# Performance work log

Measured on AMD Instinct MI355X. Metric: run time of the kernel, lower is better.

Reference implementation:

```python
import jax, jax.numpy as jnp
import numpy as np

N_HEADS = 16


def _rope(x, cos, sin):
    # x: (B,H,S,hd); cos,sin: (1,1,S,hd//2). Full-dim rotation (rot_dim == head_dim).
    xe = x[..., 0::2]
    xo = x[..., 1::2]
    re = xe * cos - xo * sin
    ro = xe * sin + xo * cos
    return jnp.stack([re, ro], axis=-1).reshape(x.shape)


def setup_inputs() -> dict:
    key = jax.random.key(0)
    B, S, D = 2, 2048, 1024
    hd = D // N_HEADS
    k1, k2, k3, k4, k5 = jax.random.split(key, 5)
    x = jax.random.normal(k1, (B, S, D), dtype=jnp.float32)
    # Linear params (lecun-normal-ish scale)
    w_qkv = jax.random.normal(k2, (D, 3 * D), dtype=jnp.float32) / np.sqrt(D)
    b_qkv = jnp.zeros((3 * D,), dtype=jnp.float32)
    w_out = jax.random.normal(k3, (D, D), dtype=jnp.float32) / np.sqrt(D)
    b_out = jnp.zeros((D,), dtype=jnp.float32)
    # Rotary tables: (S, hd//2)
    inv_freq = 1.0 / (10000.0 ** (np.arange(0, hd, 2, dtype=np.float32) / hd))
    angles = jnp.asarray(np.arange(S, dtype=np.float32)[:, None] * inv_freq[None, :])
    cos = jnp.cos(angles)
    sin = jnp.sin(angles)
    # Causal mask (seq, seq), True = attend
    mask = jnp.tril(jnp.ones((S, S), dtype=bool))
    return {"x": x, "w_qkv": w_qkv, "b_qkv": b_qkv, "w_out": w_out,
            "b_out": b_out, "cos": cos, "sin": sin, "mask": mask}


def reference(x, w_qkv, b_qkv, w_out, b_out, cos, sin, mask):
    B, S, D = x.shape
    H = N_HEADS
    hd = D // H
    scale = hd ** (-0.5)
    qkv = x @ w_qkv + b_qkv  # (B,S,3D)
    qkv = qkv.reshape(B, S, 3, H, hd).transpose(2, 0, 3, 1, 4)  # (3,B,H,S,hd)
    q, k, v = qkv[0], qkv[1], qkv[2]
    c = cos[None, None, :, :]
    s = sin[None, None, :, :]
    q = _rope(q, c, s)
    k = _rope(k, c, s)
    attn = jnp.einsum('bhqd,bhkd->bhqk', q, k) * scale
    attn = jnp.where(mask, attn, -1e9)
    attn = jax.nn.softmax(attn, axis=-1)
    out = jnp.einsum('bhqk,bhkd->bhqd', attn, v)
    out = out.transpose(0, 2, 1, 3).reshape(B, S, D)
    return out @ w_out + b_out
```

## Files before the change

kernel.cpp:

```cpp
#include <hip/hip_runtime.h>
#include <stdint.h>

typedef unsigned short u16;
typedef __attribute__((ext_vector_type(8))) __bf16 bf16x8;
typedef __attribute__((ext_vector_type(4))) float f32x4;
typedef __attribute__((ext_vector_type(4))) unsigned short u16x4;

__device__ __forceinline__ float bf2f(u16 u){
  unsigned int x = ((unsigned int)u) << 16;
  return __builtin_bit_cast(float, x);
}
__device__ __forceinline__ u16 f2bf(float f){
  return __builtin_bit_cast(u16, (__bf16)f);
}
__device__ __forceinline__ float fexp2(float x){ return __builtin_exp2f(x); }
__device__ __forceinline__ void lds_load16(const void* g, void* l){
  __builtin_amdgcn_global_load_lds(
      (const __attribute__((address_space(1))) unsigned int*)g,
      (__attribute__((address_space(3))) unsigned int*)l, 16, 0, 0);
}

__device__ __forceinline__ void transpose_body(const float* __restrict__ in,
                                               u16* __restrict__ out,
                                               int R, int C, int bx, int by,
                                               u16 (*t)[65]){
  const int c0 = bx * 64, r0 = by * 64;
  const int tid = threadIdx.x;
  const int rr = tid >> 3;
  const int cc = (tid & 7) * 8;
#pragma unroll
  for (int i = 0; i < 2; i++){
    int r = i * 32 + rr;
    const float* p = in + (size_t)(r0 + r) * C + c0 + cc;
    f32x4 v0 = *(const f32x4*)p;
    f32x4 v1 = *(const f32x4*)(p + 4);
#pragma unroll
    for (int j = 0; j < 4; j++){ t[r][cc + j] = f2bf(v0[j]); t[r][cc + 4 + j] = f2bf(v1[j]); }
  }
  __syncthreads();
#pragma unroll
  for (int i = 0; i < 2; i++){
    int c = i * 32 + rr;
    u16 tmp[8];
#pragma unroll
    for (int j = 0; j < 8; j++) tmp[j] = t[cc + j][c];
    *(bf16x8*)(out + (size_t)(c0 + c) * R + r0 + cc) = *(const bf16x8*)tmp;
  }
}

__global__ __launch_bounds__(256) void prep(const float* __restrict__ w_qkv,
                                            const float* __restrict__ w_out,
                                            const float* __restrict__ x,
                                            u16* __restrict__ wT1,
                                            u16* __restrict__ wT2,
                                            u16* __restrict__ xbf){
  __shared__ u16 t[64][65];
  const int bid = blockIdx.x;
  if (bid < 2048){
    int i = bid * 256 + threadIdx.x;
    const float* p = x + (size_t)i * 8;
    f32x4 v0 = *(const f32x4*)p;
    f32x4 v1 = *(const f32x4*)(p + 4);
    u16 tmp[8];
#pragma unroll
    for (int j = 0; j < 4; j++){ tmp[j] = f2bf(v0[j]); tmp[4 + j] = f2bf(v1[j]); }
    *(bf16x8*)(xbf + (size_t)i * 8) = *(const bf16x8*)tmp;
  } else if (bid < 2048 + 768){
    int idx = bid - 2048;
    transpose_body(w_qkv, wT1, 1024, 3072, idx % 48, idx / 48, t);
  } else {
    int idx = bid - 2816;
    transpose_body(w_out, wT2, 1024, 1024, idx % 16, idx / 16, t);
  }
}

__global__ __launch_bounds__(256) void v_transpose(const u16* __restrict__ qkv,
                                                   u16* __restrict__ vT){
  const int S = 2048, LD = 3072;
  __shared__ u16 t[64][65];
  const int bh = blockIdx.y;
  const int b = bh >> 4, h = bh & 15;
  const int s0 = blockIdx.x * 64;
  const u16* src = qkv + (size_t)b * S * LD + 2048 + h * 64;
  const int tid = threadIdx.x;
  const int rr = tid >> 3;
  const int cc = (tid & 7) * 8;
#pragma unroll
  for (int i = 0; i < 2; i++){
    int s = i * 32 + rr;
    bf16x8 v = *(const bf16x8*)(src + (size_t)(s0 + s) * LD + cc);
#pragma unroll
    for (int j = 0; j < 8; j++) t[s][cc + j] = __builtin_bit_cast(u16, (__bf16)v[j]);
  }
  __syncthreads();
  u16* dst = vT + (size_t)bh * 64 * S;
#pragma unroll
  for (int i = 0; i < 2; i++){
    int d = i * 32 + rr;
    u16 tmp[8];
#pragma unroll
    for (int j = 0; j < 8; j++) tmp[j] = t[cc + j][d];
    *(bf16x8*)(dst + (size_t)d * S + s0 + cc) = *(const bf16x8*)tmp;
  }
}

#define GSTAGE(P_, K0_)                                                        \
  { _Pragma("unroll")                                                          \
    for (int i = 0; i < 2; i++){                                               \
      int row0 = i * 64 + w * 16;                                              \
      int row = row0 + lrow;                                                   \
      int cs = lcd ^ ((row >> 1) & 3);                                         \
      lds_load16(A  + (size_t)(bm * 128 + row) * K + (K0_) + cs * 8,           \
                 (char*)As + (P_) * 8192 + row0 * 64);                         \
      lds_load16(Bt + (size_t)(bn * 128 + row) * K + (K0_) + cs * 8,           \
                 (char*)Bs + (P_) * 8192 + row0 * 64);                         \
    } }

template<bool OUTF32, bool ROPE>
__global__ __launch_bounds__(256, 3) void gemm_bt(const u16* __restrict__ A,
                                                  const u16* __restrict__ Bt,
                                                  const float* __restrict__ bias,
                                                  void* __restrict__ Cv,
                                                  int M, int N, int K,
                                                  const float* __restrict__ cosb,
                                                  const float* __restrict__ sinb,
                                                  u16* __restrict__ vTo){
  __shared__ u16 smem[16384];
  u16* As = smem;
  u16* Bs = smem + 8192;
  const int nx = gridDim.x;
  const int L = blockIdx.x + nx * blockIdx.y;
  const int per = (nx * gridDim.y) >> 3;
  const int wg = (L & 7) * per + (L >> 3);
  const int bn = wg % nx, bm = wg / nx;
  const int tid = threadIdx.x, w = tid >> 6, l = tid & 63;
  const int lo = l & 15, hi = l >> 4;
  const int wr = (w >> 1) * 64, wc = (w & 1) * 64;
  f32x4 acc[4][4] = {};
  const int lrow = l >> 2, lcd = l & 3;

  GSTAGE(0, 0);
  __syncthreads();
  for (int k0 = 0; k0 < K; k0 += 32){
    const int p = (k0 >> 5) & 1;
    if (k0 + 32 < K) GSTAGE(p ^ 1, k0 + 32);
    bf16x8 a[4], b[4];
#pragma unroll
    for (int mi = 0; mi < 4; mi++){
      int row = wr + mi * 16 + lo;
      unsigned byte = (unsigned)(row * 64 + hi * 16) ^ (((row >> 1) & 3) << 4);
      a[mi] = *(const bf16x8*)((const char*)As + p * 8192 + byte);
    }
#pragma unroll
    for (int ni = 0; ni < 4; ni++){
      int row = wc + ni * 16 + lo;
      unsigned byte = (unsigned)(row * 64 + hi * 16) ^ (((row >> 1) & 3) << 4);
      b[ni] = *(const bf16x8*)((const char*)Bs + p * 8192 + byte);
    }
    __builtin_amdgcn_s_setprio(1);
#pragma unroll
    for (int mi = 0; mi < 4; mi++)
#pragma unroll
      for (int ni = 0; ni < 4; ni++)
        acc[mi][ni] = __builtin_amdgcn_mfma_f32_16x16x32_bf16(a[mi], b[ni], acc[mi][ni], 0, 0, 0);
    __builtin_amdgcn_s_setprio(0);
    __syncthreads();
  }
  if (ROPE && bn < 16){
#pragma unroll
    for (int mi = 0; mi < 4; mi++){
#pragma unroll
      for (int r = 0; r < 4; r++){
        int grow = bm * 128 + wr + mi * 16 + hi * 4 + r;
        int stok = grow & 2047;
#pragma unroll
        for (int ni = 0; ni < 4; ni++){
          int col = bn * 128 + wc + ni * 16 + lo;
          float v = acc[mi][ni][r] + bias[col];
          float partner = __shfl_xor(v, 1, 64);
          int ip = (col & 63) >> 1;
          float c = cosb[stok * 32 + ip], sn = sinb[stok * 32 + ip];
          float res = (lo & 1) ? (partner * sn + v * c) : (v * c - partner * sn);
          ((u16*)Cv)[(size_t)grow * N + col] = f2bf(res);
        }
      }
    }
  } else if (ROPE && vTo != nullptr){
    const int bloc = (bm * 128) >> 11;
    const int s0g  = (bm * 128) & 2047;
#pragma unroll
    for (int H = 0; H < 2; H++){
      if ((w & 1) == H){
#pragma unroll
        for (int mi = 0; mi < 4; mi++){
#pragma unroll
          for (int ni = 0; ni < 4; ni++){
            int d = ni * 16 + lo;
            int col = bn * 128 + wc + ni * 16 + lo;
            int sb = wr + mi * 16 + hi * 4;
            u16x4 pk;
#pragma unroll
            for (int r = 0; r < 4; r++) pk[r] = f2bf(acc[mi][ni][r] + bias[col]);
            *(u16x4*)&smem[d * 128 + (sb ^ ((d & 15) << 3))] = pk;
          }
        }
      }
      __syncthreads();
      int hh = (bn - 16) * 2 + H;
      u16* dst = vTo + (size_t)(bloc * 16 + hh) * 64 * 2048;
#pragma unroll
      for (int i = 0; i < 4; i++){
        int c = tid + 256 * i;
        int d = c >> 4, sc = c & 15;
        bf16x8 v = *(const bf16x8*)&smem[d * 128 + ((sc * 8) ^ ((d & 15) << 3))];
        *(bf16x8*)(dst + (size_t)d * 2048 + s0g + sc * 8) = v;
      }
      __syncthreads();
    }
  } else {
#pragma unroll
    for (int mi = 0; mi < 4; mi++){
#pragma unroll
      for (int r = 0; r < 4; r++){
        int grow = bm * 128 + wr + mi * 16 + hi * 4 + r;
#pragma unroll
        for (int ni = 0; ni < 4; ni++){
          int col = bn * 128 + wc + ni * 16 + lo;
          float v = acc[mi][ni][r] + bias[col];
          if (OUTF32)
            ((float*)Cv)[(size_t)grow * N + col] = v;
          else
            ((u16*)Cv)[(size_t)grow * N + col] = f2bf(v);
        }
      }
    }
  }
}

#define FA_DSREAD(KB_, KT_)                                                    \
  { _Pragma("unroll")                                                          \
    for (int c = 0; c < 2; c++){                                               \
      _Pragma("unroll")                                                        \
      for (int f = 0; f < 2; f++){                                             \
        int srw = f * 16 + lo;                                                 \
        unsigned byte = ((unsigned)(srw * 128 + c * 64 + hi * 16)) ^           \
                        ((lo & 7) << 4);                                       \
        KB_[c * 2 + f] = *(const bf16x8*)(                                     \
            (const char*)&Ks[w][(KT_) & 1][0] + byte);                         \
      } } }

#define FA_STAGE(KT_)                                                          \
  { _Pragma("unroll")                                                          \
    for (int i = 0; i < 4; i++)                                                \
      lds_load16(Kp + (size_t)((KT_) * 32 + i * 8 + srow8) * LD + scs * 8,     \
                 (char*)&Ks[w][(KT_) & 1][0] + i * 1024); }

#define FA_BODY(KBU_, KBL_, KT_, OA_, OB_, MA_, MB_)                           \
  {                                                                            \
    bf16x8 vb[4];                                                              \
    _Pragma("unroll")                                                          \
    for (int fd = 0; fd < 4; fd++)                                             \
      vb[fd] = *(const bf16x8*)(Vb + (size_t)(fd * 16 + lo) * S +              \
                                (KT_) * 32 + hi * 8);                          \
    if ((KT_) + 1 < k1) FA_DSREAD(KBL_, (KT_) + 1);                            \
    f32x4 saA[2] = {}, saB[2] = {};                                            \
    __builtin_amdgcn_s_setprio(1);                                             \
    saA[0] = __builtin_amdgcn_mfma_f32_16x16x32_bf16(KBU_[0], qfA0, saA[0], 0, 0, 0); \
    saB[0] = __builtin_amdgcn_mfma_f32_16x16x32_bf16(KBU_[0], qfB0, saB[0], 0, 0, 0); \
    saA[0] = __builtin_amdgcn_mfma_f32_16x16x32_bf16(KBU_[2], qfA1, saA[0], 0, 0, 0); \
    saB[0] = __builtin_amdgcn_mfma_f32_16x16x32_bf16(KBU_[2], qfB1, saB[0], 0, 0, 0); \
    saA[1] = __builtin_amdgcn_mfma_f32_16x16x32_bf16(KBU_[1], qfA0, saA[1], 0, 0, 0); \
    saB[1] = __builtin_amdgcn_mfma_f32_16x16x32_bf16(KBU_[1], qfB0, saB[1], 0, 0, 0); \
    saA[1] = __builtin_amdgcn_mfma_f32_16x16x32_bf16(KBU_[3], qfA1, saA[1], 0, 0, 0); \
    saB[1] = __builtin_amdgcn_mfma_f32_16x16x32_bf16(KBU_[3], qfB1, saB[1], 0, 0, 0); \
    __builtin_amdgcn_s_setprio(0);                                             \
    __builtin_amdgcn_sched_barrier(0);                                         \
    if ((KT_) + 2 < k1) FA_STAGE((KT_) + 2);                                   \
    if ((KT_) == nkt - 1){                                                     \
      _Pragma("unroll")                                                        \
      for (int f = 0; f < 2; f++){                                             \
        int key0 = (KT_) * 32 + f * 16 + hi * 4;                               \
        _Pragma("unroll")                                                      \
        for (int r = 0; r < 4; r++){                                           \
          if (key0 + r > qrA) saA[f][r] = -1e30f;                              \
          if (key0 + r > qrB) saB[f][r] = -1e30f;                              \
        }                                                                      \
      }                                                                        \
    }                                                                          \
    float pmA = fmaxf(                                                         \
        fmaxf(fmaxf(saA[0][0], saA[0][1]), fmaxf(saA[0][2], saA[0][3])),       \
        fmaxf(fmaxf(saA[1][0], saA[1][1]), fmaxf(saA[1][2], saA[1][3])));      \
    float pmB = fmaxf(                                                         \
        fmaxf(fmaxf(saB[0][0], saB[0][1]), fmaxf(saB[0][2], saB[0][3])),       \
        fmaxf(fmaxf(saB[1][0], saB[1][1]), fmaxf(saB[1][2], saB[1][3])));      \
    if (!__all(fmaxf(pmA - MA_, pmB - MB_) <= 11.5f)){                         \
      float rmA = fmaxf(pmA, __shfl_xor(pmA, 16, 64));                         \
      rmA = fmaxf(rmA, __shfl_xor(rmA, 32, 64));                               \
      float rmB = fmaxf(pmB, __shfl_xor(pmB, 16, 64));                         \
      rmB = fmaxf(rmB, __shfl_xor(rmB, 32, 64));                               \
      float mnA = fmaxf(MA_, rmA), mnB = fmaxf(MB_, rmB);                      \
      float cA = fexp2(MA_ - mnA), cB = fexp2(MB_ - mnB);                      \
      MA_ = mnA; MB_ = mnB;                                                    \
      lparA *= cA; lparB *= cB;                                                \
      float cqA[4], cqB[4];                                                    \
      _Pragma("unroll")                                                        \
      for (int r = 0; r < 4; r++){                                             \
        cqA[r] = __shfl(cA, hi * 4 + r, 64);                                   \
        cqB[r] = __shfl(cB, hi * 4 + r, 64);                                   \
      }                                                                        \
      _Pragma("unroll")                                                        \
      for (int fd = 0; fd < 4; fd++){                                          \
        _Pragma("unroll")                                                      \
        for (int r = 0; r < 4; r++){                                           \
          OA_[fd][r] *= cqA[r]; OB_[fd][r] *= cqB[r];                          \
        }                                                                      \
      }                                                                        \
    }                                                                          \
    float pvA[2][4], pvB[2][4];                                                \
    _Pragma("unroll")                                                          \
    for (int f = 0; f < 2; f++){                                               \
      _Pragma("unroll")                                                        \
      for (int r = 0; r < 4; r++){                                             \
        pvA[f][r] = fexp2(saA[f][r] - MA_);                                    \
        pvB[f][r] = fexp2(saB[f][r] - MB_);                                    \
      }                                                                        \
    }                                                                          \
    _Pragma("unroll")                                                          \
    for (int f = 0; f < 2; f++){                                               \
      u16x4 pkA, pkB;                                                          \
      _Pragma("unroll")                                                        \
      for (int r = 0; r < 4; r++){                                             \
        pkA[r] = f2bf(pvA[f][r]); pkB[r] = f2bf(pvB[f][r]);                    \
      }                                                                        \
      *(u16x4*)((char*)&Ps[w][0][0] + lo * 72 + f * 32 + hi * 8) = pkA;        \
      *(u16x4*)((char*)&Ps[w][1][0] + lo * 72 + f * 32 + hi * 8) = pkB;        \
    }                                                                          \
    lparA += ((pvA[0][0] + pvA[0][1]) + (pvA[0][2] + pvA[0][3]))               \
           + ((pvA[1][0] + pvA[1][1]) + (pvA[1][2] + pvA[1][3]));              \
    lparB += ((pvB[0][0] + pvB[0][1]) + (pvB[0][2] + pvB[0][3]))               \
           + ((pvB[1][0] + pvB[1][1]) + (pvB[1][2] + pvB[1][3]));              \
    bf16x8 paA = *(const bf16x8*)((const char*)&Ps[w][0][0] + lo * 72 +        \
                                  hi * 16);                                    \
    bf16x8 paB = *(const bf16x8*)((const char*)&Ps[w][1][0] + lo * 72 +        \
                                  hi * 16);                                    \
    __builtin_amdgcn_s_setprio(1);                                             \
    _Pragma("unroll")                                                          \
    for (int fd = 0; fd < 4; fd++){                                            \
      OA_[fd] = __builtin_amdgcn_mfma_f32_16x16x32_bf16(paA, vb[fd],           \
                                                        OA_[fd], 0, 0, 0);     \
      OB_[fd] = __builtin_amdgcn_mfma_f32_16x16x32_bf16(paB, vb[fd],           \
                                                        OB_[fd], 0, 0, 0);     \
    }                                                                          \
    __builtin_amdgcn_s_setprio(0);                                             \
  }

#define FA_PHASE(T_, OA_, OB_, MA_, MB_, LA_, LB_)                             \
  {                                                                            \
    const int q0p = (T_) * 32;                                                 \
    const int qrA = q0p + lo, qrB = q0p + 16 + lo;                             \
    const int nkt = (T_) + 1;                                                  \
    const int ch = (nkt + 1) >> 1;                                             \
    const int k0 = w ? ch : 0;                                                 \
    const int k1 = w ? nkt : ch;                                               \
    bf16x8 qfA0, qfA1, qfB0, qfB1;                                             \
    {                                                                          \
      bf16x8 va0 = *(const bf16x8*)(Qp + (size_t)qrA * LD + hi * 8);           \
      bf16x8 va1 = *(const bf16x8*)(Qp + (size_t)qrA * LD + 32 + hi * 8);      \
      bf16x8 vb0 = *(const bf16x8*)(Qp + (size_t)qrB * LD + hi * 8);           \
      bf16x8 vb1 = *(const bf16x8*)(Qp + (size_t)qrB * LD + 32 + hi * 8);      \
      _Pragma("unroll")                                                        \
      for (int j = 0; j < 8; j++){                                             \
        qfA0[j] = (__bf16)((float)va0[j] * QSC);                               \
        qfA1[j] = (__bf16)((float)va1[j] * QSC);                               \
        qfB0[j] = (__bf16)((float)vb0[j] * QSC);                               \
        qfB1[j] = (__bf16)((float)vb1[j] * QSC);                               \
      }                                                                        \
    }                                                                          \
    float lparA = 0.f, lparB = 0.f;                                            \
    MA_ = -1e30f; MB_ = -1e30f;                                                \
    bf16x8 kbA[4], kbB[4];                                                     \
    int kt = k0;                                                               \
    if (kt < k1){                                                              \
      FA_STAGE(kt);                                                            \
      if (kt + 1 < k1) FA_STAGE(kt + 1);                                       \
      FA_DSREAD(kbA, kt);                                                      \
      while (true){                                                            \
        FA_BODY(kbA, kbB, kt, OA_, OB_, MA_, MB_);                             \
        kt++;                                                                  \
        if (kt >= k1) break;                                                   \
        FA_BODY(kbB, kbA, kt, OA_, OB_, MA_, MB_);                             \
        kt++;                                                                  \
        if (kt >= k1) break;                                                   \
      }                                                                        \
    }                                                                          \
    lparA += __shfl_xor(lparA, 16, 64); lparA += __shfl_xor(lparA, 32, 64);    \
    lparB += __shfl_xor(lparB, 16, 64); lparB += __shfl_xor(lparB, 32, 64);    \
    LA_ = lparA; LB_ = lparB;                                                  \
  }

#define FA_WRITEPART(slot_, OA_, OB_, MA_, MB_, LA_, LB_)                      \
  {                                                                            \
    _Pragma("unroll")                                                          \
    for (int fd = 0; fd < 4; fd++){                                            \
      u16x4 pkA, pkB;                                                          \
      _Pragma("unroll")                                                        \
      for (int r = 0; r < 4; r++){                                             \
        pkA[r] = f2bf(OA_[fd][r]); pkB[r] = f2bf(OB_[fd][r]);                  \
      }                                                                        \
      *(u16x4*)((char*)&Xo[slot_][0] + (fd * 16 + lo) * 72 + hi * 8) = pkA;    \
      *(u16x4*)((char*)&Xo[slot_][0] + (fd * 16 + lo) * 72 + 32 + hi * 8) = pkB;\
    }                                                                          \
    if (hi == 0){                                                              \
      Xm[slot_][lo] = MA_;      Xl[slot_][lo] = LA_;                           \
      Xm[slot_][16 + lo] = MB_; Xl[slot_][16 + lo] = LB_;                      \
    }                                                                          \
  }

#define FA_COMBINE(slot_, T_, OA_, OB_, MA_, MB_, LA_, LB_)                    \
  {                                                                            \
    const int q0p = (T_) * 32;                                                 \
    u16x4 pA[4], pB[4];                                                        \
    _Pragma("unroll")                                                          \
    for (int fd = 0; fd < 4; fd++){                                            \
      pA[fd] = *(const u16x4*)((const char*)&Xo[slot_][0] +                    \
                               (fd * 16 + lo) * 72 + hi * 8);                  \
      pB[fd] = *(const u16x4*)((const char*)&Xo[slot_][0] +                    \
                               (fd * 16 + lo) * 72 + 32 + hi * 8);             \
    }                                                                          \
    _Pragma("unroll")                                                          \
    for (int r = 0; r < 4; r++){                                               \
      float mOA = __shfl(MA_, hi * 4 + r, 64);                                 \
      float lOA = __shfl(LA_, hi * 4 + r, 64);                                 \
      float mOB = __shfl(MB_, hi * 4 + r, 64);                                 \
      float lOB = __shfl(LB_, hi * 4 + r, 64);                                 \
      float mPA = Xm[slot_][hi * 4 + r], lPA = Xl[slot_][hi * 4 + r];          \
      float mPB = Xm[slot_][16 + hi * 4 + r], lPB = Xl[slot_][16 + hi * 4 + r];\
      float MfA = fmaxf(mOA, mPA), MfB = fmaxf(mOB, mPB);                      \
      float c0A = fexp2(mOA - MfA), c1A = fexp2(mPA - MfA);                    \
      float c0B = fexp2(mOB - MfB), c1B = fexp2(mPB - MfB);                    \
      float invA = 1.0f / (lOA * c0A + lPA * c1A);                             \
      float invB = 1.0f / (lOB * c0B + lPB * c1B);                             \
      int srA = q0p + hi * 4 + r;                                              \
      int srB = q0p + 16 + hi * 4 + r;                                         \
      u16* orA = Oout + (size_t)(b * S + srA) * 1024 + h * 64;                 \
      u16* orB = Oout + (size_t)(b * S + srB) * 1024 + h * 64;                 \
      _Pragma("unroll")                                                        \
      for (int fd = 0; fd < 4; fd++){                                          \
        float vA = (OA_[fd][r] * c0A + bf2f(pA[fd][r]) * c1A) * invA;          \
        float vB = (OB_[fd][r] * c0B + bf2f(pB[fd][r]) * c1B) * invB;          \
        orA[fd * 16 + lo] = f2bf(vA);                                          \
        orB[fd * 16 + lo] = f2bf(vB);                                          \
      }                                                                        \
    }                                                                          \
  }

__global__ __launch_bounds__(128, 2) void flash_attn(const u16* __restrict__ qkv,
                                                     const u16* __restrict__ vT,
                                                     u16* __restrict__ Oout){
  const int S = 2048, LD = 3072;
  const int L = blockIdx.x;
  const int bh = L & 31;
  const int bx = L >> 5;
  const int b = bh >> 4, h = bh & 15;
  const u16* base = qkv + (size_t)b * S * LD;
  const u16* Qp = base + h * 64;
  const u16* Kp = base + 1024 + h * 64;
  const u16* Vb = vT + (size_t)bh * 64 * S;
  const int tid = threadIdx.x, w = tid >> 6, l = tid & 63;
  const int lo = l & 15, hi = l >> 4;
  __shared__ u16 Ks[2][2][32 * 64];
  __shared__ u16 Ps[2][2][16 * 36];
  __shared__ u16 Xo[2][64 * 36];
  __shared__ float Xm[2][32], Xl[2][32];

  const float QSC = 0.125f * 1.44269504089f;
  const int srow8 = l >> 3;
  const int scs = (l & 7) ^ srow8;

  f32x4 o1A[4] = {}, o1B[4] = {};
  f32x4 o2A[4] = {}, o2B[4] = {};
  float m1A, m1B, l1A, l1B, m2A, m2B, l2A, l2B;

  FA_PHASE(63 - bx, o1A, o1B, m1A, m1B, l1A, l1B);
  if (w == 1) FA_WRITEPART(0, o1A, o1B, m1A, m1B, l1A, l1B);
  FA_PHASE(bx,      o2A, o2B, m2A, m2B, l2A, l2B);
  if (w == 0) FA_WRITEPART(1, o2A, o2B, m2A, m2B, l2A, l2B);
  __syncthreads();
  if (w == 0){
    FA_COMBINE(0, 63 - bx, o1A, o1B, m1A, m1B, l1A, l1B);
  } else {
    FA_COMBINE(1, bx,      o2A, o2B, m2A, m2B, l2A, l2B);
  }
}

extern "C" void kernel_launch(void* const* d_in, const int* in_sizes, int n_in,
                              void* d_out, int out_size, void* d_ws, size_t ws_size,
                              hipStream_t stream){
  const float* x     = (const float*)d_in[0];
  const float* w_qkv = (const float*)d_in[1];
  const float* b_qkv = (const float*)d_in[2];
  const float* w_out = (const float*)d_in[3];
  const float* b_out = (const float*)d_in[4];
  const float* cosb  = (const float*)d_in[5];
  const float* sinb  = (const float*)d_in[6];
  float* out = (float*)d_out;
  char* ws = (char*)d_ws;
  u16* qkv  = (u16*)(ws);
  u16* attn = (u16*)(ws + 25165824);
  u16* xbf  = attn;
  u16* wT2  = (u16*)(ws + 33554432);
  u16* wT1  = (u16*)(ws + 35651584);

  const bool fuse = ws_size >= (size_t)50331648;
  u16* vT = fuse ? (u16*)(ws + 41943040)
                 : (u16*)(ws + 35651584);

  prep<<<3072, 256, 0, stream>>>(w_qkv, w_out, x, wT1, wT2, xbf);
  gemm_bt<false, true ><<<dim3(24, 32), 256, 0, stream>>>(
      xbf, wT1, b_qkv, qkv, 4096, 3072, 1024, cosb, sinb, fuse ? vT : nullptr);
  if (!fuse)
    v_transpose<<<dim3(32, 32), 256, 0, stream>>>(qkv, vT);
  flash_attn<<<1024, 128, 0, stream>>>(qkv, vT, attn);
  gemm_bt<true , false><<<dim3(8, 32), 256, 0, stream>>>(
      attn, wT2, b_out, out, 4096, 1024, 1024, cosb, sinb, nullptr);
}
```

Baseline: 115.2 us.

## Process two key tiles per flash-attention iteration with a widened P buffer

Restructures the flash-attention inner loop to handle 64 keys (two 32-key tiles) per iteration. The loop now issues both tiles' K LDS reads and V global loads up front, runs one row-max/rescale check for both tiles, and stages the next two K tiles together. A single-tile body handles an odd tail. The P scratch buffer is doubled so both tiles' probabilities can be staged, which halves the per-tile softmax reduction and branch overhead. The trade-offs are the loss of the earlier one-tile-ahead K register prefetch, higher register pressure, and more LDS use.

```diff
diff --git a/kernel.cpp b/kernel.cpp
--- a/kernel.cpp
+++ b/kernel.cpp
@@ -255,27 +255,144 @@
       lds_load16(Kp + (size_t)((KT_) * 32 + i * 8 + srow8) * LD + scs * 8,     \
                  (char*)&Ks[w][(KT_) & 1][0] + i * 1024); }
 
-#define FA_BODY(KBU_, KBL_, KT_, OA_, OB_, MA_, MB_)                           \
+#define FA_RESCALE(PMA_, PMB_, OA_, OB_, MA_, MB_)                             \
+    if (!__all(fmaxf((PMA_) - MA_, (PMB_) - MB_) <= 11.5f)){                   \
+      float rmA = fmaxf(PMA_, __shfl_xor(PMA_, 16, 64));                       \
+      rmA = fmaxf(rmA, __shfl_xor(rmA, 32, 64));                               \
+      float rmB = fmaxf(PMB_, __shfl_xor(PMB_, 16, 64));                       \
+      rmB = fmaxf(rmB, __shfl_xor(rmB, 32, 64));                               \
+      float mnA = fmaxf(MA_, rmA), mnB = fmaxf(MB_, rmB);                      \
+      float cA = fexp2(MA_ - mnA), cB = fexp2(MB_ - mnB);                      \
+      MA_ = mnA; MB_ = mnB;                                                    \
+      lparA *= cA; lparB *= cB;                                                \
+      float cqA[4], cqB[4];                                                    \
+      _Pragma("unroll")                                                        \
+      for (int r = 0; r < 4; r++){                                             \
+        cqA[r] = __shfl(cA, hi * 4 + r, 64);                                   \
+        cqB[r] = __shfl(cB, hi * 4 + r, 64);                                   \
+      }                                                                        \
+      _Pragma("unroll")                                                        \
+      for (int fd = 0; fd < 4; fd++){                                          \
+        _Pragma("unroll")                                                      \
+        for (int r = 0; r < 4; r++){                                           \
+          OA_[fd][r] *= cqA[r]; OB_[fd][r] *= cqB[r];                          \
+        }                                                                      \
+      }                                                                        \
+    }
+
+#define PM8(sa) fmaxf(fmaxf(fmaxf(sa[0][0], sa[0][1]), fmaxf(sa[0][2], sa[0][3])), \
+                      fmaxf(fmaxf(sa[1][0], sa[1][1]), fmaxf(sa[1][2], sa[1][3])))
+
+#define FA_BODY2(KT_, OA_, OB_, MA_, MB_)                                      \
   {                                                                            \
-    bf16x8 vb[4];                                                              \
-    _Pragma("unroll")                                                          \
-    for (int fd = 0; fd < 4; fd++)                                             \
-      vb[fd] = *(const bf16x8*)(Vb + (size_t)(fd * 16 + lo) * S +              \
-                                (KT_) * 32 + hi * 8);                          \
-    if ((KT_) + 1 < k1) FA_DSREAD(KBL_, (KT_) + 1);                            \
-    f32x4 saA[2] = {}, saB[2] = {};                                            \
+    bf16x8 kb0[4], kb1[4];                                                     \
+    FA_DSREAD(kb0, KT_);                                                       \
+    FA_DSREAD(kb1, (KT_) + 1);                                                 \
+    bf16x8 vb0[4], vb1[4];                                                     \
+    _Pragma("unroll")                                                          \
+    for (int fd = 0; fd < 4; fd++){                                            \
+      vb0[fd] = *(const bf16x8*)(Vb + (size_t)(fd * 16 + lo) * S +             \
+                                 (KT_) * 32 + hi * 8);                         \
+      vb1[fd] = *(const bf16x8*)(Vb + (size_t)(fd * 16 + lo) * S +             \
+                                 ((KT_) + 1) * 32 + hi * 8);                   \
+    }                                                                          \
+    f32x4 saA0[2] = {}, saA1[2] = {}, saB0[2] = {}, saB1[2] = {};              \
     __builtin_amdgcn_s_setprio(1);                                             \
-    saA[0] = __builtin_amdgcn_mfma_f32_16x16x32_bf16(KBU_[0], qfA0, saA[0], 0, 0, 0); \
-    saB[0] = __builtin_amdgcn_mfma_f32_16x16x32_bf16(KBU_[0], qfB0, saB[0], 0, 0, 0); \
-    saA[0] = __builtin_amdgcn_mfma_f32_16x16x32_bf16(KBU_[2], qfA1, saA[0], 0, 0, 0); \
-    saB[0] = __builtin_amdgcn_mfma_f32_16x16x32_bf16(KBU_[2], qfB1, saB[0], 0, 0, 0); \
-    saA[1] = __builtin_amdgcn_mfma_f32_16x16x32_bf16(KBU_[1], qfA0, saA[1], 0, 0, 0); \
-    saB[1] = __builtin_amdgcn_mfma_f32_16x16x32_bf16(KBU_[1], qfB0, saB[1], 0, 0, 0); \
-    saA[1] = __builtin_amdgcn_mfma_f32_16x16x32_bf16(KBU_[3], qfA1, saA[1], 0, 0, 0); \
-    saB[1] = __builtin_amdgcn_mfma_f32_16x16x32_bf16(KBU_[3], qfB1, saB[1], 0, 0, 0); \
+    _Pragma("unroll")                                                          \
+    for (int f = 0; f < 2; f++){                                               \
+      saA0[f] = __builtin_amdgcn_mfma_f32_16x16x32_bf16(kb0[f],     qfA0, saA0[f], 0, 0, 0); \
+      saB0[f] = __builtin_amdgcn_mfma_f32_16x16x32_bf16(kb0[f],     qfB0, saB0[f], 0, 0, 0); \
+      saA0[f] = __builtin_amdgcn_mfma_f32_16x16x32_bf16(kb0[2 + f], qfA1, saA0[f], 0, 0, 0); \
+      saB0[f] = __builtin_amdgcn_mfma_f32_16x16x32_bf16(kb0[2 + f], qfB1, saB0[f], 0, 0, 0); \
+      saA1[f] = __builtin_amdgcn_mfma_f32_16x16x32_bf16(kb1[f],     qfA0, saA1[f], 0, 0, 0); \
+      saB1[f] = __builtin_amdgcn_mfma_f32_16x16x32_bf16(kb1[f],     qfB0, saB1[f], 0, 0, 0); \
+      saA1[f] = __builtin_amdgcn_mfma_f32_16x16x32_bf16(kb1[2 + f], qfA1, saA1[f], 0, 0, 0); \
+      saB1[f] = __builtin_amdgcn_mfma_f32_16x16x32_bf16(kb1[2 + f], qfB1, saB1[f], 0, 0, 0); \
+    }                                                                          \
     __builtin_amdgcn_s_setprio(0);                                             \
     __builtin_amdgcn_sched_barrier(0);                                         \
     if ((KT_) + 2 < k1) FA_STAGE((KT_) + 2);                                   \
+    if ((KT_) + 3 < k1) FA_STAGE((KT_) + 3);                                   \
+    if ((KT_) + 1 == nkt - 1){                                                 \
+      _Pragma("unroll")                                                        \
+      for (int f = 0; f < 2; f++){                                             \
+        int key0 = ((KT_) + 1) * 32 + f * 16 + hi * 4;                         \
+        _Pragma("unroll")                                                      \
+        for (int r = 0; r < 4; r++){                                           \
+          if (key0 + r > qrA) saA1[f][r] = -1e30f;                             \
+          if (key0 + r > qrB) saB1[f][r] = -1e30f;                             \
+        }                                                                      \
+      }                                                                        \
+    }                                                                          \
+    float pmA = fmaxf(PM8(saA0), PM8(saA1));                                   \
+    float pmB = fmaxf(PM8(saB0), PM8(saB1));                                   \
+    FA_RESCALE(pmA, pmB, OA_, OB_, MA_, MB_);                                  \
+    float pvA0[2][4], pvA1[2][4], pvB0[2][4], pvB1[2][4];                      \
+    _Pragma("unroll")                                                          \
+    for (int f = 0; f < 2; f++){                                               \
+      _Pragma("unroll")                                                        \
+      for (int r = 0; r < 4; r++){                                             \
+        pvA0[f][r] = fexp2(saA0[f][r] - MA_);                                  \
+        pvA1[f][r] = fexp2(saA1[f][r] - MA_);                                  \
+        pvB0[f][r] = fexp2(saB0[f][r] - MB_);                                  \
+        pvB1[f][r] = fexp2(saB1[f][r] - MB_);                                  \
+      }                                                                        \
+    }                                                                          \
+    _Pragma("unroll")                                                          \
+    for (int f = 0; f < 2; f++){                                               \
+      u16x4 pkA0, pkA1, pkB0, pkB1;                                            \
+      _Pragma("unroll")                                                        \
+      for (int r = 0; r < 4; r++){                                             \
+        pkA0[r] = f2bf(pvA0[f][r]); pkA1[r] = f2bf(pvA1[f][r]);                \
+        pkB0[r] = f2bf(pvB0[f][r]); pkB1[r] = f2bf(pvB1[f][r]);                \
+      }                                                                        \
+      *(u16x4*)((char*)&Ps[w][0][0] + lo * 144 + f * 32 + hi * 8) = pkA0;      \
+      *(u16x4*)((char*)&Ps[w][0][0] + lo * 144 + 64 + f * 32 + hi * 8) = pkA1; \
+      *(u16x4*)((char*)&Ps[w][1][0] + lo * 144 + f * 32 + hi * 8) = pkB0;      \
+      *(u16x4*)((char*)&Ps[w][1][0] + lo * 144 + 64 + f * 32 + hi * 8) = pkB1; \
+    }                                                                          \
+    lparA += (((pvA0[0][0] + pvA0[0][1]) + (pvA0[0][2] + pvA0[0][3]))          \
+            + ((pvA0[1][0] + pvA0[1][1]) + (pvA0[1][2] + pvA0[1][3])))         \
+           + (((pvA1[0][0] + pvA1[0][1]) + (pvA1[0][2] + pvA1[0][3]))          \
+            + ((pvA1[1][0] + pvA1[1][1]) + (pvA1[1][2] + pvA1[1][3])));        \
+    lparB += (((pvB0[0][0] + pvB0[0][1]) + (pvB0[0][2] + pvB0[0][3]))          \
+            + ((pvB0[1][0] + pvB0[1][1]) + (pvB0[1][2] + pvB0[1][3])))         \
+           + (((pvB1[0][0] + pvB1[0][1]) + (pvB1[0][2] + pvB1[0][3]))          \
+            + ((pvB1[1][0] + pvB1[1][1]) + (pvB1[1][2] + pvB1[1][3])));        \
+    bf16x8 paA0 = *(const bf16x8*)((const char*)&Ps[w][0][0] + lo * 144 + hi * 16);      \
+    bf16x8 paA1 = *(const bf16x8*)((const char*)&Ps[w][0][0] + lo * 144 + 64 + hi * 16); \
+    bf16x8 paB0 = *(const bf16x8*)((const char*)&Ps[w][1][0] + lo * 144 + hi * 16);      \
+    bf16x8 paB1 = *(const bf16x8*)((const char*)&Ps[w][1][0] + lo * 144 + 64 + hi * 16); \
+    __builtin_amdgcn_s_setprio(1);                                             \
+    _Pragma("unroll")                                                          \
+    for (int fd = 0; fd < 4; fd++){                                            \
+      OA_[fd] = __builtin_amdgcn_mfma_f32_16x16x32_bf16(paA0, vb0[fd], OA_[fd], 0, 0, 0); \
+      OB_[fd] = __builtin_amdgcn_mfma_f32_16x16x32_bf16(paB0, vb0[fd], OB_[fd], 0, 0, 0); \
+      OA_[fd] = __builtin_amdgcn_mfma_f32_16x16x32_bf16(paA1, vb1[fd], OA_[fd], 0, 0, 0); \
+      OB_[fd] = __builtin_amdgcn_mfma_f32_16x16x32_bf16(paB1, vb1[fd], OB_[fd], 0, 0, 0); \
+    }                                                                          \
+    __builtin_amdgcn_s_setprio(0);                                             \
+  }
+
+#define FA_BODY1(KT_, OA_, OB_, MA_, MB_)                                      \
+  {                                                                            \
+    bf16x8 kbt[4];                                                             \
+    FA_DSREAD(kbt, KT_);                                                       \
+    bf16x8 vbt[4];                                                             \
+    _Pragma("unroll")                                                          \
+    for (int fd = 0; fd < 4; fd++)                                             \
+      vbt[fd] = *(const bf16x8*)(Vb + (size_t)(fd * 16 + lo) * S +             \
+                                 (KT_) * 32 + hi * 8);                         \
+    f32x4 saA[2] = {}, saB[2] = {};                                            \
+    __builtin_amdgcn_s_setprio(1);                                             \
+    _Pragma("unroll")                                                          \
+    for (int f = 0; f < 2; f++){                                               \
+      saA[f] = __builtin_amdgcn_mfma_f32_16x16x32_bf16(kbt[f],     qfA0, saA[f], 0, 0, 0); \
+      saB[f] = __builtin_amdgcn_mfma_f32_16x16x32_bf16(kbt[f],     qfB0, saB[f], 0, 0, 0); \
+      saA[f] = __builtin_amdgcn_mfma_f32_16x16x32_bf16(kbt[2 + f], qfA1, saA[f], 0, 0, 0); \
+      saB[f] = __builtin_amdgcn_mfma_f32_16x16x32_bf16(kbt[2 + f], qfB1, saB[f], 0, 0, 0); \
+    }                                                                          \
+    __builtin_amdgcn_s_setprio(0);                                             \
     if ((KT_) == nkt - 1){                                                     \
       _Pragma("unroll")                                                        \
       for (int f = 0; f < 2; f++){                                             \
@@ -287,35 +404,9 @@
         }                                                                      \
       }                                                                        \
     }                                                                          \
-    float pmA = fmaxf(                                                         \
-        fmaxf(fmaxf(saA[0][0], saA[0][1]), fmaxf(saA[0][2], saA[0][3])),       \
-        fmaxf(fmaxf(saA[1][0], saA[1][1]), fmaxf(saA[1][2], saA[1][3])));      \
-    float pmB = fmaxf(                                                         \
-        fmaxf(fmaxf(saB[0][0], saB[0][1]), fmaxf(saB[0][2], saB[0][3])),       \
-        fmaxf(fmaxf(saB[1][0], saB[1][1]), fmaxf(saB[1][2], saB[1][3])));      \
-    if (!__all(fmaxf(pmA - MA_, pmB - MB_) <= 11.5f)){                         \
-      float rmA = fmaxf(pmA, __shfl_xor(pmA, 16, 64));                         \
-      rmA = fmaxf(rmA, __shfl_xor(rmA, 32, 64));                               \
-      float rmB = fmaxf(pmB, __shfl_xor(pmB, 16, 64));                         \
-      rmB = fmaxf(rmB, __shfl_xor(rmB, 32, 64));                               \
-      float mnA = fmaxf(MA_, rmA), mnB = fmaxf(MB_, rmB);                      \
-      float cA = fexp2(MA_ - mnA), cB = fexp2(MB_ - mnB);                      \
-      MA_ = mnA; MB_ = mnB;                                                    \
-      lparA *= cA; lparB *= cB;                                                \
-      float cqA[4], cqB[4];                                                    \
-      _Pragma("unroll")                                                        \
-      for (int r = 0; r < 4; r++){                                             \
-        cqA[r] = __shfl(cA, hi * 4 + r, 64);                                   \
-        cqB[r] = __shfl(cB, hi * 4 + r, 64);                                   \
-      }                                                                        \
-      _Pragma("unroll")                                                        \
-      for (int fd = 0; fd < 4; fd++){                                          \
-        _Pragma("unroll")                                                      \
-        for (int r = 0; r < 4; r++){                                           \
-          OA_[fd][r] *= cqA[r]; OB_[fd][r] *= cqB[r];                          \
-        }                                                                      \
-      }                                                                        \
-    }                                                                          \
+    float pmA = PM8(saA);                                                      \
+    float pmB = PM8(saB);                                                      \
+    FA_RESCALE(pmA, pmB, OA_, OB_, MA_, MB_);                                  \
     float pvA[2][4], pvB[2][4];                                                \
     _Pragma("unroll")                                                          \
     for (int f = 0; f < 2; f++){                                               \
@@ -332,24 +423,20 @@
       for (int r = 0; r < 4; r++){                                             \
         pkA[r] = f2bf(pvA[f][r]); pkB[r] = f2bf(pvB[f][r]);                    \
       }                                                                        \
-      *(u16x4*)((char*)&Ps[w][0][0] + lo * 72 + f * 32 + hi * 8) = pkA;        \
-      *(u16x4*)((char*)&Ps[w][1][0] + lo * 72 + f * 32 + hi * 8) = pkB;        \
+      *(u16x4*)((char*)&Ps[w][0][0] + lo * 144 + f * 32 + hi * 8) = pkA;       \
+      *(u16x4*)((char*)&Ps[w][1][0] + lo * 144 + f * 32 + hi * 8) = pkB;       \
     }                                                                          \
     lparA += ((pvA[0][0] + pvA[0][1]) + (pvA[0][2] + pvA[0][3]))               \
            + ((pvA[1][0] + pvA[1][1]) + (pvA[1][2] + pvA[1][3]));              \
     lparB += ((pvB[0][0] + pvB[0][1]) + (pvB[0][2] + pvB[0][3]))               \
            + ((pvB[1][0] + pvB[1][1]) + (pvB[1][2] + pvB[1][3]));              \
-    bf16x8 paA = *(const bf16x8*)((const char*)&Ps[w][0][0] + lo * 72 +        \
-                                  hi * 16);                                    \
-    bf16x8 paB = *(const bf16x8*)((const char*)&Ps[w][1][0] + lo * 72 +        \
-                                  hi * 16);                                    \
+    bf16x8 paA = *(const bf16x8*)((const char*)&Ps[w][0][0] + lo * 144 + hi * 16); \
+    bf16x8 paB = *(const bf16x8*)((const char*)&Ps[w][1][0] + lo * 144 + hi * 16); \
     __builtin_amdgcn_s_setprio(1);                                             \
     _Pragma("unroll")                                                          \
     for (int fd = 0; fd < 4; fd++){                                            \
-      OA_[fd] = __builtin_amdgcn_mfma_f32_16x16x32_bf16(paA, vb[fd],           \
-                                                        OA_[fd], 0, 0, 0);     \
-      OB_[fd] = __builtin_amdgcn_mfma_f32_16x16x32_bf16(paB, vb[fd],           \
-                                                        OB_[fd], 0, 0, 0);     \
+      OA_[fd] = __builtin_amdgcn_mfma_f32_16x16x32_bf16(paA, vbt[fd], OA_[fd], 0, 0, 0); \
+      OB_[fd] = __builtin_amdgcn_mfma_f32_16x16x32_bf16(paB, vbt[fd], OB_[fd], 0, 0, 0); \
     }                                                                          \
     __builtin_amdgcn_s_setprio(0);                                             \
   }
@@ -378,19 +465,16 @@
     }                                                                          \
     float lparA = 0.f, lparB = 0.f;                                            \
     MA_ = -1e30f; MB_ = -1e30f;                                                \
-    bf16x8 kbA[4], kbB[4];                                                     \
     int kt = k0;                                                               \
     if (kt < k1){                                                              \
       FA_STAGE(kt);                                                            \
       if (kt + 1 < k1) FA_STAGE(kt + 1);                                       \
-      FA_DSREAD(kbA, kt);                                                      \
-      while (true){                                                            \
-        FA_BODY(kbA, kbB, kt, OA_, OB_, MA_, MB_);                             \
-        kt++;                                                                  \
-        if (kt >= k1) break;                                                   \
-        FA_BODY(kbB, kbA, kt, OA_, OB_, MA_, MB_);                             \
-        kt++;                                                                  \
-        if (kt >= k1) break;                                                   \
+      while (kt + 1 < k1){                                                     \
+        FA_BODY2(kt, OA_, OB_, MA_, MB_);                                      \
+        kt += 2;                                                               \
+      }                                                                        \
+      if (kt < k1){                                                            \
+        FA_BODY1(kt, OA_, OB_, MA_, MB_);                                      \
       }                                                                        \
     }                                                                          \
     lparA += __shfl_xor(lparA, 16, 64); lparA += __shfl_xor(lparA, 32, 64);    \
@@ -469,7 +553,7 @@
   const int tid = threadIdx.x, w = tid >> 6, l = tid & 63;
   const int lo = l & 15, hi = l >> 4;
   __shared__ u16 Ks[2][2][32 * 64];
-  __shared__ u16 Ps[2][2][16 * 36];
+  __shared__ u16 Ps[2][2][16 * 72];
   __shared__ u16 Xo[2][64 * 36];
   __shared__ float Xm[2][32], Xl[2][32];
 
```

Result: no change. 116.3 us (+1.0%).
